# Performance work log

Hardware: AMD Instinct MI355X
Metric: run time of the kernel (lower is better)

Reference implementation:

```python
import jax, jax.numpy as jnp
import numpy as np

H = 2048      # hidden_dim
P = 256       # private_subspace_dim
B, S = 4, 8192


def setup_inputs() -> dict:
    key = jax.random.key(0)
    k1, k2, k3, k4, k5 = jax.random.split(key, 5)
    hidden_states = jax.random.normal(k1, (B, S, H), dtype=jnp.float32)
    token_ids = jax.random.randint(k2, (B, S), 0, 100, dtype=jnp.int32)
    # Linear params (torch nn.Linear: y = x @ W.T + b); store W as (in, out) for einsum.
    sc1 = 1.0 / np.sqrt(H)
    sc2 = 1.0 / np.sqrt(P)
    W_to = jax.random.uniform(k3, (H, P), jnp.float32, -sc1, sc1)
    b_to = jnp.zeros((P,), jnp.float32)
    W_from = jax.random.uniform(k4, (P, H), jnp.float32, -sc2, sc2)
    b_from = jnp.zeros((H,), jnp.float32)
    return {
        "hidden_states": hidden_states,
        "W_to": W_to, "b_to": b_to,
        "W_from": W_from, "b_from": b_from,
        "token_ids": token_ids,
        "thought_token_id": 5,
    }


def _thought_mask(token_ids, thought_token_id):
    # Replaces the sequential toggle loop: state at position i is the parity of the
    # number of thought tokens seen in token_ids[0, :i+1] (toggle happens BEFORE use).
    matches = (token_ids[0] == thought_token_id).astype(jnp.int32)   # (S,)
    parity = (jnp.cumsum(matches) % 2) == 1                          # (S,) bool
    return jnp.broadcast_to(parity[None, :], token_ids.shape)        # (B, S)


def reference(hidden_states, W_to, b_to, W_from, b_from, token_ids, thought_token_id):
    is_private = _thought_mask(token_ids, thought_token_id)          # (B, S) bool
    m = is_private.astype(hidden_states.dtype)[..., None]            # (B, S, 1)
    private_reasoning = jnp.einsum('bsh,hp->bsp', hidden_states, W_to) + b_to
    private_projected = jnp.einsum('bsp,ph->bsh', private_reasoning, W_from) + b_from
    output = hidden_states * (1.0 - m) + private_projected * m
    subspace_usage = is_private.astype(jnp.float32).mean(axis=1)     # (B,)
    return private_reasoning, output, is_private, subspace_usage
```

## Files before the change

### kernel.cpp

```cpp
#include <hip/hip_runtime.h>
#include <stdint.h>


#define H 2048
#define P 256
#define BB 4
#define S 8192
#define M_TOTAL (BB * S)

typedef __bf16 bf16x8 __attribute__((ext_vector_type(8)));
typedef float f32x4 __attribute__((ext_vector_type(4)));

__device__ __forceinline__ ushort f2b(float f) {
  uint32_t u = __float_as_uint(f);
  u += 0x7fffu + ((u >> 16) & 1u);
  return (ushort)(u >> 16);
}

__global__ void mask_kernel(const int* __restrict__ tok, const int* __restrict__ tt_p,
                            float* __restrict__ maskf, float* __restrict__ out2,
                            float* __restrict__ out3) {
  __shared__ int segpar[256];
  __shared__ int segcnt[256];
  __shared__ int totalsh;
  const int t = threadIdx.x;
  const int tt = tt_p[0];
  const int base = t * 32;
  unsigned bits = 0;
  for (int i = 0; i < 32; i++) bits |= (unsigned)(tok[base + i] == tt) << i;
  segpar[t] = __popc(bits) & 1;
  __syncthreads();
  int pre = 0;
  for (int j = 0; j < t; j++) pre ^= segpar[j];
  int cnt = 0;
  for (int i = 0; i < 32; i++) {
    int inc = __popc(bits & (0xFFFFFFFFu >> (31 - i))) & 1;
    int bit = pre ^ inc;
    cnt += bit;
    float fb = (float)bit;
    maskf[base + i] = fb;
    out2[0 * S + base + i] = fb;
    out2[1 * S + base + i] = fb;
    out2[2 * S + base + i] = fb;
    out2[3 * S + base + i] = fb;
  }
  segcnt[t] = cnt;
  __syncthreads();
  if (t == 0) {
    int tot = 0;
    for (int j = 0; j < 256; j++) tot += segcnt[j];
    totalsh = tot;
  }
  __syncthreads();
  if (t < BB) out3[t] = (float)totalsh / (float)S;
}

__global__ void transpose_cvt(const float* __restrict__ in, ushort* __restrict__ out,
                              int R, int C) {
  __shared__ float tile[32][33];
  const int c0 = blockIdx.x * 32, r0 = blockIdx.y * 32;
  const int tx = threadIdx.x, ty = threadIdx.y;
#pragma unroll
  for (int j = 0; j < 32; j += 8)
    tile[ty + j][tx] = in[(size_t)(r0 + ty + j) * C + c0 + tx];
  __syncthreads();
#pragma unroll
  for (int j = 0; j < 32; j += 8)
    out[(size_t)(c0 + ty + j) * R + r0 + tx] = f2b(tile[tx][ty + j]);
}

__global__ __launch_bounds__(512) void fused_main(
    const float* __restrict__ hid,
    const ushort* __restrict__ wtT,
    const ushort* __restrict__ wfT,
    const float* __restrict__ b_to,
    const float* __restrict__ b_from,
    const float* __restrict__ maskf,
    float* __restrict__ out0,
    float* __restrict__ out1)
{
  __shared__ ushort sPR[128 * 264];
  __shared__ ushort scratch[33792];
  ushort* sA = scratch;
  ushort* sW = scratch + 128 * 72;
  ushort* sWf = scratch;

  const int tid = threadIdx.x;
  const int lane = tid & 63, wid = tid >> 6;
  const int quad = lane >> 4, l16 = lane & 15;
  const int row0 = blockIdx.x * 128;

  const int wrA = wid >> 2;
  const int wcA = wid & 3;
  f32x4 acc[4][4];
  const f32x4 zero = {0.f, 0.f, 0.f, 0.f};
#pragma unroll
  for (int i = 0; i < 4; i++)
#pragma unroll
    for (int j = 0; j < 4; j++) acc[i][j] = zero;

  for (int k0 = 0; k0 < H; k0 += 64) {
#pragma unroll
    for (int p = 0; p < 4; p++) {
      int u = p * 512 + tid;
      int r = u >> 4, cc = u & 15;
      const float4 v = *(const float4*)(hid + (size_t)(row0 + r) * H + k0 + cc * 4);
      ushort4 b;
      b.x = f2b(v.x); b.y = f2b(v.y); b.z = f2b(v.z); b.w = f2b(v.w);
      *(ushort4*)(sA + r * 72 + cc * 4) = b;
    }
#pragma unroll
    for (int p = 0; p < 4; p++) {
      int u = p * 512 + tid;
      int n = u >> 3, s = u & 7;
      *(int4*)(sW + n * 72 + s * 8) = *(const int4*)(wtT + (size_t)n * H + k0 + s * 8);
    }
    __syncthreads();
#pragma unroll
    for (int kk = 0; kk < 64; kk += 32) {
      bf16x8 af[4], bfr[4];
#pragma unroll
      for (int t = 0; t < 4; t++)
        af[t] = *(const bf16x8*)(sA + (wrA * 64 + t * 16 + l16) * 72 + kk + quad * 8);
#pragma unroll
      for (int t = 0; t < 4; t++)
        bfr[t] = *(const bf16x8*)(sW + (wcA * 64 + t * 16 + l16) * 72 + kk + quad * 8);
#pragma unroll
      for (int i = 0; i < 4; i++)
#pragma unroll
        for (int j = 0; j < 4; j++)
          acc[i][j] = __builtin_amdgcn_mfma_f32_16x16x32_bf16(af[i], bfr[j], acc[i][j], 0, 0, 0);
    }
    __syncthreads();
  }

#pragma unroll
  for (int i = 0; i < 4; i++) {
#pragma unroll
    for (int j = 0; j < 4; j++) {
      int col = wcA * 64 + j * 16 + l16;
      float bias = b_to[col];
#pragma unroll
      for (int e = 0; e < 4; e++) {
        int row = wrA * 64 + i * 16 + quad * 4 + e;
        float v = acc[i][j][e] + bias;
        out0[(size_t)(row0 + row) * P + col] = v;
        sPR[row * 264 + col] = f2b(v);
      }
    }
  }

  const int wrB = wid >> 1;
  const int wcB = wid & 1;

  for (int nc = 0; nc < H; nc += 128) {
#pragma unroll
    for (int p = 0; p < 8; p++) {
      int u = p * 512 + tid;
      int n = u >> 5, s = u & 31;
      *(int4*)(sWf + n * 264 + s * 8) = *(const int4*)(wfT + (size_t)(nc + n) * P + s * 8);
    }
    __syncthreads();
    f32x4 acc2[2][4];
#pragma unroll
    for (int i = 0; i < 2; i++)
#pragma unroll
      for (int j = 0; j < 4; j++) acc2[i][j] = zero;
#pragma unroll
    for (int kk = 0; kk < P; kk += 32) {
      bf16x8 af[2], bfr[4];
#pragma unroll
      for (int t = 0; t < 2; t++)
        af[t] = *(const bf16x8*)(sPR + (wrB * 32 + t * 16 + l16) * 264 + kk + quad * 8);
#pragma unroll
      for (int t = 0; t < 4; t++)
        bfr[t] = *(const bf16x8*)(sWf + (wcB * 64 + t * 16 + l16) * 264 + kk + quad * 8);
#pragma unroll
      for (int i = 0; i < 2; i++)
#pragma unroll
        for (int j = 0; j < 4; j++)
          acc2[i][j] = __builtin_amdgcn_mfma_f32_16x16x32_bf16(af[i], bfr[j], acc2[i][j], 0, 0, 0);
    }
    __syncthreads();

#pragma unroll
    for (int i = 0; i < 2; i++) {
#pragma unroll
      for (int e = 0; e < 4; e++) {
        int row = wrB * 32 + i * 16 + quad * 4 + e;
        size_t gr = (size_t)(row0 + row);
        float m = maskf[gr & (S - 1)];
#pragma unroll
        for (int j = 0; j < 4; j++) {
          int col = nc + wcB * 64 + j * 16 + l16;
          float v = acc2[i][j][e] + b_from[col];
          float o = (m != 0.0f) ? v : hid[gr * H + col];
          out1[gr * H + col] = o;
        }
      }
    }
  }
}

extern "C" void kernel_launch(void* const* d_in, const int* in_sizes, int n_in,
                              void* d_out, int out_size, void* d_ws, size_t ws_size,
                              hipStream_t stream) {
  const float* hid    = (const float*)d_in[0];
  const float* W_to   = (const float*)d_in[1];
  const float* b_to   = (const float*)d_in[2];
  const float* W_from = (const float*)d_in[3];
  const float* b_from = (const float*)d_in[4];
  const int*   tok    = (const int*)d_in[5];
  const int*   tt     = (const int*)d_in[6];

  ushort* wtT = (ushort*)d_ws;
  ushort* wfT = wtT + (size_t)P * H;
  float* maskf = (float*)(wfT + (size_t)H * P);

  float* out0 = (float*)d_out;
  float* out1 = out0 + (size_t)BB * S * P;
  float* out2 = out1 + (size_t)BB * S * H;
  float* out3 = out2 + (size_t)BB * S;

  hipLaunchKernelGGL(mask_kernel, dim3(1), dim3(256), 0, stream, tok, tt, maskf, out2, out3);
  hipLaunchKernelGGL(transpose_cvt, dim3(P / 32, H / 32), dim3(32, 8), 0, stream, W_to, wtT, H, P);
  hipLaunchKernelGGL(transpose_cvt, dim3(H / 32, P / 32), dim3(32, 8), 0, stream, W_from, wfT, P, H);
  hipLaunchKernelGGL(fused_main, dim3(M_TOTAL / 128), dim3(512), 0, stream,
                     hid, wtT, wfT, b_to, b_from, maskf, out0, out1);
}
```

Before: 749.3 us.

## Split fused two-GEMM kernel into separate GEMM launches and warp-level mask scan

Splits the fused kernel into two launches. gemm1 computes private_reasoning with 64-row tiles, which doubles the grid. gemm2 reads out0 back from global memory and tiles the output over both M and N with a block-index swizzle, giving far more blocks and better parallelism. The mask kernel now uses wave ballots and shuffles in place of serial shared-memory scans. The trade-off is an extra global round trip of the fp32 intermediate and a second launch, in exchange for higher occupancy and shorter per-block serial work.

```diff
diff --git a/kernel.cpp b/kernel.cpp
--- a/kernel.cpp
+++ b/kernel.cpp
@@ -20,21 +20,24 @@
 __global__ void mask_kernel(const int* __restrict__ tok, const int* __restrict__ tt_p,
                             float* __restrict__ maskf, float* __restrict__ out2,
                             float* __restrict__ out3) {
-  __shared__ int segpar[256];
-  __shared__ int segcnt[256];
-  __shared__ int totalsh;
+  __shared__ unsigned long long wpar[4];
+  __shared__ int wcnt[4];
   const int t = threadIdx.x;
+  const int lane = t & 63, w = t >> 6;
   const int tt = tt_p[0];
   const int base = t * 32;
   unsigned bits = 0;
   for (int i = 0; i < 32; i++) bits |= (unsigned)(tok[base + i] == tt) << i;
-  segpar[t] = __popc(bits) & 1;
+  const int par = __popc(bits) & 1;
+  const unsigned long long bal = __ballot(par != 0);
+  if (lane == 0) wpar[w] = bal;
   __syncthreads();
   int pre = 0;
-  for (int j = 0; j < t; j++) pre ^= segpar[j];
+  for (int j = 0; j < w; j++) pre ^= (int)(__popcll(wpar[j]) & 1);
+  pre ^= (int)(__popcll(bal & ((1ull << lane) - 1ull)) & 1);
   int cnt = 0;
   for (int i = 0; i < 32; i++) {
-    int inc = __popc(bits & (0xFFFFFFFFu >> (31 - i))) & 1;
+    int inc = __popc(bits << (31 - i)) & 1;
     int bit = pre ^ inc;
     cnt += bit;
     float fb = (float)bit;
@@ -44,15 +47,13 @@
     out2[2 * S + base + i] = fb;
     out2[3 * S + base + i] = fb;
   }
-  segcnt[t] = cnt;
+  for (int off = 32; off; off >>= 1) cnt += __shfl_down(cnt, off);
+  if (lane == 0) wcnt[w] = cnt;
   __syncthreads();
-  if (t == 0) {
-    int tot = 0;
-    for (int j = 0; j < 256; j++) tot += segcnt[j];
-    totalsh = tot;
-  }
-  __syncthreads();
-  if (t < BB) out3[t] = (float)totalsh / (float)S;
+  if (t < BB) {
+    int tot = wcnt[0] + wcnt[1] + wcnt[2] + wcnt[3];
+    out3[t] = (float)tot / (float)S;
+  }
 }
 
 __global__ void transpose_cvt(const float* __restrict__ in, ushort* __restrict__ out,
@@ -69,39 +70,29 @@
     out[(size_t)(c0 + ty + j) * R + r0 + tx] = f2b(tile[tx][ty + j]);
 }
 
-__global__ __launch_bounds__(512) void fused_main(
+__global__ __launch_bounds__(512) void gemm1(
     const float* __restrict__ hid,
     const ushort* __restrict__ wtT,
-    const ushort* __restrict__ wfT,
     const float* __restrict__ b_to,
-    const float* __restrict__ b_from,
-    const float* __restrict__ maskf,
-    float* __restrict__ out0,
-    float* __restrict__ out1)
+    float* __restrict__ out0)
 {
-  __shared__ ushort sPR[128 * 264];
-  __shared__ ushort scratch[33792];
-  ushort* sA = scratch;
-  ushort* sW = scratch + 128 * 72;
-  ushort* sWf = scratch;
-
+  __shared__ ushort sA[64 * 72];
+  __shared__ ushort sW[256 * 72];
   const int tid = threadIdx.x;
   const int lane = tid & 63, wid = tid >> 6;
   const int quad = lane >> 4, l16 = lane & 15;
-  const int row0 = blockIdx.x * 128;
-
-  const int wrA = wid >> 2;
-  const int wcA = wid & 3;
-  f32x4 acc[4][4];
+  const int row0 = blockIdx.x * 64;
+
+  f32x4 acc[4][2];
   const f32x4 zero = {0.f, 0.f, 0.f, 0.f};
 #pragma unroll
   for (int i = 0; i < 4; i++)
 #pragma unroll
-    for (int j = 0; j < 4; j++) acc[i][j] = zero;
+    for (int j = 0; j < 2; j++) acc[i][j] = zero;
 
   for (int k0 = 0; k0 < H; k0 += 64) {
 #pragma unroll
-    for (int p = 0; p < 4; p++) {
+    for (int p = 0; p < 2; p++) {
       int u = p * 512 + tid;
       int r = u >> 4, cc = u & 15;
       const float4 v = *(const float4*)(hid + (size_t)(row0 + r) * H + k0 + cc * 4);
@@ -118,15 +109,93 @@
     __syncthreads();
 #pragma unroll
     for (int kk = 0; kk < 64; kk += 32) {
-      bf16x8 af[4], bfr[4];
+      bf16x8 af[4], bfr[2];
 #pragma unroll
       for (int t = 0; t < 4; t++)
-        af[t] = *(const bf16x8*)(sA + (wrA * 64 + t * 16 + l16) * 72 + kk + quad * 8);
+        af[t] = *(const bf16x8*)(sA + (t * 16 + l16) * 72 + kk + quad * 8);
+#pragma unroll
+      for (int t = 0; t < 2; t++)
+        bfr[t] = *(const bf16x8*)(sW + (wid * 32 + t * 16 + l16) * 72 + kk + quad * 8);
+#pragma unroll
+      for (int i = 0; i < 4; i++)
+#pragma unroll
+        for (int j = 0; j < 2; j++)
+          acc[i][j] = __builtin_amdgcn_mfma_f32_16x16x32_bf16(af[i], bfr[j], acc[i][j], 0, 0, 0);
+    }
+    __syncthreads();
+  }
+
+#pragma unroll
+  for (int i = 0; i < 4; i++) {
+#pragma unroll
+    for (int j = 0; j < 2; j++) {
+      int col = wid * 32 + j * 16 + l16;
+      float bias = b_to[col];
+#pragma unroll
+      for (int e = 0; e < 4; e++) {
+        int row = i * 16 + quad * 4 + e;
+        out0[(size_t)(row0 + row) * P + col] = acc[i][j][e] + bias;
+      }
+    }
+  }
+}
+
+__global__ __launch_bounds__(512) void gemm2(
+    const float* __restrict__ pr,
+    const ushort* __restrict__ wfT,
+    const float* __restrict__ b_from,
+    const float* __restrict__ maskf,
+    const float* __restrict__ hid,
+    float* __restrict__ out1)
+{
+  __shared__ ushort sA[128 * 72];
+  __shared__ ushort sW[128 * 72];
+  const int tid = threadIdx.x;
+  const int lane = tid & 63, wid = tid >> 6;
+  const int quad = lane >> 4, l16 = lane & 15;
+
+  const int u0 = (blockIdx.x & 7) * 512 + (blockIdx.x >> 3);
+  const int mblk = u0 >> 4, nblk = u0 & 15;
+  const int row0 = mblk * 128, nc0 = nblk * 128;
+
+  const int wr = wid >> 1;
+  const int wc = wid & 1;
+
+  f32x4 acc[2][4];
+  const f32x4 zero = {0.f, 0.f, 0.f, 0.f};
+#pragma unroll
+  for (int i = 0; i < 2; i++)
+#pragma unroll
+    for (int j = 0; j < 4; j++) acc[i][j] = zero;
+
+  for (int k0 = 0; k0 < P; k0 += 64) {
+#pragma unroll
+    for (int p = 0; p < 4; p++) {
+      int u = p * 512 + tid;
+      int r = u >> 4, cc = u & 15;
+      const float4 v = *(const float4*)(pr + (size_t)(row0 + r) * P + k0 + cc * 4);
+      ushort4 b;
+      b.x = f2b(v.x); b.y = f2b(v.y); b.z = f2b(v.z); b.w = f2b(v.w);
+      *(ushort4*)(sA + r * 72 + cc * 4) = b;
+    }
+#pragma unroll
+    for (int p = 0; p < 2; p++) {
+      int u = p * 512 + tid;
+      int n = u >> 3, s = u & 7;
+      *(int4*)(sW + n * 72 + s * 8) = *(const int4*)(wfT + (size_t)(nc0 + n) * P + k0 + s * 8);
+    }
+    __syncthreads();
+#pragma unroll
+    for (int kk = 0; kk < 64; kk += 32) {
+      bf16x8 af[2], bfr[4];
+#pragma unroll
+      for (int t = 0; t < 2; t++)
+        af[t] = *(const bf16x8*)(sA + (wr * 32 + t * 16 + l16) * 72 + kk + quad * 8);
 #pragma unroll
       for (int t = 0; t < 4; t++)
-        bfr[t] = *(const bf16x8*)(sW + (wcA * 64 + t * 16 + l16) * 72 + kk + quad * 8);
-#pragma unroll
-      for (int i = 0; i < 4; i++)
+        bfr[t] = *(const bf16x8*)(sW + (wc * 64 + t * 16 + l16) * 72 + kk + quad * 8);
+#pragma unroll
+      for (int i = 0; i < 2; i++)
 #pragma unroll
         for (int j = 0; j < 4; j++)
           acc[i][j] = __builtin_amdgcn_mfma_f32_16x16x32_bf16(af[i], bfr[j], acc[i][j], 0, 0, 0);
@@ -135,67 +204,23 @@
   }
 
 #pragma unroll
-  for (int i = 0; i < 4; i++) {
-#pragma unroll
-    for (int j = 0; j < 4; j++) {
-      int col = wcA * 64 + j * 16 + l16;
-      float bias = b_to[col];
-#pragma unroll
-      for (int e = 0; e < 4; e++) {
-        int row = wrA * 64 + i * 16 + quad * 4 + e;
-        float v = acc[i][j][e] + bias;
-        out0[(size_t)(row0 + row) * P + col] = v;
-        sPR[row * 264 + col] = f2b(v);
-      }
-    }
-  }
-
-  const int wrB = wid >> 1;
-  const int wcB = wid & 1;
-
-  for (int nc = 0; nc < H; nc += 128) {
-#pragma unroll
-    for (int p = 0; p < 8; p++) {
-      int u = p * 512 + tid;
-      int n = u >> 5, s = u & 31;
-      *(int4*)(sWf + n * 264 + s * 8) = *(const int4*)(wfT + (size_t)(nc + n) * P + s * 8);
-    }
-    __syncthreads();
-    f32x4 acc2[2][4];
-#pragma unroll
-    for (int i = 0; i < 2; i++)
-#pragma unroll
-      for (int j = 0; j < 4; j++) acc2[i][j] = zero;
-#pragma unroll
-    for (int kk = 0; kk < P; kk += 32) {
-      bf16x8 af[2], bfr[4];
-#pragma unroll
-      for (int t = 0; t < 2; t++)
-        af[t] = *(const bf16x8*)(sPR + (wrB * 32 + t * 16 + l16) * 264 + kk + quad * 8);
-#pragma unroll
-      for (int t = 0; t < 4; t++)
-        bfr[t] = *(const bf16x8*)(sWf + (wcB * 64 + t * 16 + l16) * 264 + kk + quad * 8);
-#pragma unroll
-      for (int i = 0; i < 2; i++)
-#pragma unroll
-        for (int j = 0; j < 4; j++)
-          acc2[i][j] = __builtin_amdgcn_mfma_f32_16x16x32_bf16(af[i], bfr[j], acc2[i][j], 0, 0, 0);
-    }
-    __syncthreads();
-
-#pragma unroll
-    for (int i = 0; i < 2; i++) {
-#pragma unroll
-      for (int e = 0; e < 4; e++) {
-        int row = wrB * 32 + i * 16 + quad * 4 + e;
-        size_t gr = (size_t)(row0 + row);
-        float m = maskf[gr & (S - 1)];
+  for (int i = 0; i < 2; i++) {
+#pragma unroll
+    for (int e = 0; e < 4; e++) {
+      int row = wr * 32 + i * 16 + quad * 4 + e;
+      size_t gr = (size_t)(row0 + row);
+      float m = maskf[gr & (S - 1)];
+      if (m != 0.0f) {
 #pragma unroll
         for (int j = 0; j < 4; j++) {
-          int col = nc + wcB * 64 + j * 16 + l16;
-          float v = acc2[i][j][e] + b_from[col];
-          float o = (m != 0.0f) ? v : hid[gr * H + col];
-          out1[gr * H + col] = o;
+          int col = nc0 + wc * 64 + j * 16 + l16;
+          out1[gr * H + col] = acc[i][j][e] + b_from[col];
+        }
+      } else {
+#pragma unroll
+        for (int j = 0; j < 4; j++) {
+          int col = nc0 + wc * 64 + j * 16 + l16;
+          out1[gr * H + col] = hid[gr * H + col];
         }
       }
     }
@@ -225,6 +250,7 @@
   hipLaunchKernelGGL(mask_kernel, dim3(1), dim3(256), 0, stream, tok, tt, maskf, out2, out3);
   hipLaunchKernelGGL(transpose_cvt, dim3(P / 32, H / 32), dim3(32, 8), 0, stream, W_to, wtT, H, P);
   hipLaunchKernelGGL(transpose_cvt, dim3(H / 32, P / 32), dim3(32, 8), 0, stream, W_from, wfT, P, H);
-  hipLaunchKernelGGL(fused_main, dim3(M_TOTAL / 128), dim3(512), 0, stream,
-                     hid, wtT, wfT, b_to, b_from, maskf, out0, out1);
-}
+  hipLaunchKernelGGL(gemm1, dim3(M_TOTAL / 64), dim3(512), 0, stream, hid, wtT, b_to, out0);
+  hipLaunchKernelGGL(gemm2, dim3((M_TOTAL / 128) * (H / 128)), dim3(512), 0, stream,
+                     out0, wfT, b_from, maskf, hid, out1);
+}
```

New measurement: 669.4 us. -10.7%, faster.
